# Kernel tuning notes

Hardware: AMD Instinct MI355X
Metric: run time of the kernel (lower is better)

## Reference

```python
import jax, jax.numpy as jnp
import numpy as np

N_NODES = 20000
N_EDGES = 320000
IN_F = 256
OUT_F = 64
HEADS = 4
ALPHA = 0.1  # leaky_relu negative slope


def setup_inputs() -> dict:
    key = jax.random.key(0)
    ks = jax.random.split(key, 8)
    return {
        "input1": jax.random.normal(ks[0], (N_NODES, IN_F), jnp.float32),
        "input2": jax.random.normal(ks[1], (N_NODES, IN_F), jnp.float32),
        # per-head params: Ws maps source feats -> target_out, Wt maps target feats -> source_out
        "Ws": jax.random.normal(ks[2], (HEADS, IN_F, OUT_F), jnp.float32) * 0.06,
        "Wt": jax.random.normal(ks[3], (HEADS, IN_F, OUT_F), jnp.float32) * 0.06,
        "a1": jax.random.normal(ks[4], (HEADS, 2 * OUT_F), jnp.float32) * 0.1,
        "a2": jax.random.normal(ks[5], (HEADS, 2 * OUT_F), jnp.float32) * 0.1,
        # COO nonzeros of A_opt [n_target, n_source]
        "tgt_idx": jax.random.randint(ks[6], (N_EDGES,), 0, N_NODES),
        "src_idx": jax.random.randint(ks[7], (N_EDGES,), 0, N_NODES),
    }


def _segment_softmax(scores, seg, num_segments):
    m = jax.lax.stop_gradient(jax.ops.segment_max(scores, seg, num_segments=num_segments))
    w = jnp.exp(scores - m[seg])
    d = jax.ops.segment_sum(w, seg, num_segments=num_segments)
    d = jnp.where(d == 0, 1.0, d)
    return w / d[seg]


def _head(x1, x2, Ws, Wt, a1, a2, src, tgt, n_s, n_t):
    s = x1 @ Ws  # [n_s, OUT_F]  messages source -> target
    t = x2 @ Wt  # [n_t, OUT_F]  messages target -> source
    out = Ws.shape[1]
    # edge score e = leaky_relu(a^T [s_src || t_tgt]); split a to avoid edge-level concat
    e1 = jax.nn.leaky_relu((s @ a1[:out])[src] + (t @ a1[out:])[tgt], ALPHA)
    e2 = jax.nn.leaky_relu((s @ a2[:out])[src] + (t @ a2[out:])[tgt], ALPHA)
    alpha_ts = _segment_softmax(e1, tgt, n_t)  # softmax over sources per target
    alpha_st = _segment_softmax(e2, src, n_s)  # softmax over targets per source
    h_ts = jax.ops.segment_sum(alpha_ts[:, None] * s[src], tgt, num_segments=n_t)
    h_st = jax.ops.segment_sum(alpha_st[:, None] * t[tgt], src, num_segments=n_s)
    return jax.nn.elu(h_st), jax.nn.elu(h_ts)  # concat=True -> ELU per head


def reference(input1, input2, Ws, Wt, a1, a2, tgt_idx, src_idx):
    n_s, n_t = input1.shape[0], input2.shape[0]
    head_fn = jax.vmap(
        lambda W1, W2, v1, v2: _head(input1, input2, W1, W2, v1, v2, src_idx, tgt_idx, n_s, n_t)
    )
    h_st, h_ts = head_fn(Ws, Wt, a1, a2)  # each [H, n, OUT_F]
    h_st = jnp.transpose(h_st, (1, 0, 2)).reshape(n_s, -1)  # concat heads
    h_ts = jnp.transpose(h_ts, (1, 0, 2)).reshape(n_t, -1)
    return h_st, h_ts
```

## Files before the change

### kernel.cpp

```cpp
#include <hip/hip_runtime.h>
#include <math.h>

#define N_NODES 20000
#define N_EDGES 320000
#define IN_F 256
#define OUT_F 64
#define HEADS 4
#define NCOL 256
#define LRELU_ALPHA 0.1f
#define ELL_CAP 64

#define SCAT_BLOCKS 640
#define SCAT_THREADS (SCAT_BLOCKS * 256)

#define WRES_BLOCKS 128
#define LDS_STRIDE 264

typedef __attribute__((ext_vector_type(8))) short short8;
typedef __attribute__((ext_vector_type(4))) float floatx4;

__device__ __forceinline__ float lrelu(float x) {
    return x > 0.f ? x : LRELU_ALPHA * x;
}
__device__ __forceinline__ unsigned short f2bf(float f) {
    unsigned int u = __float_as_uint(f);
    u = (u + 0x7FFF + ((u >> 16) & 1)) >> 16;
    return (unsigned short)u;
}
__device__ __forceinline__ float bf2f(unsigned short u) {
    return __uint_as_float(((unsigned int)u) << 16);
}

__global__ __launch_bounds__(256) void prep_w_kernel(
    const float* __restrict__ Ws, const float* __restrict__ Wt,
    unsigned short* __restrict__ Wsb, unsigned short* __restrict__ Wtb,
    int* __restrict__ cnt)
{
    const int gid = blockIdx.x * 256 + threadIdx.x;

    for (int i = gid; i < 2 * N_NODES; i += 16384) cnt[i] = 0;

    const int mat = gid >> 13;
    const int r   = gid & 8191;
    const int kc  = r >> 8;
    const int c   = r & 255;
    const float* W    = mat ? Wt : Ws;
    unsigned short* O = mat ? Wtb : Wsb;
    const int h = c >> 6, j = c & 63;
    const int k0 = kc * 8;
    unsigned short v[8] __attribute__((aligned(16)));
#pragma unroll
    for (int i = 0; i < 8; ++i)
        v[i] = f2bf(W[(size_t)h * (IN_F * OUT_F) + (size_t)(k0 + i) * OUT_F + j]);
    *(uint4*)(O + (size_t)c * IN_F + k0) = *(const uint4*)v;
}

__global__ __launch_bounds__(256) void scatter_kernel(
    const int* __restrict__ src, const int* __restrict__ tgt,
    int* __restrict__ cnt_t, int* __restrict__ cnt_s,
    unsigned short* __restrict__ elist_t, unsigned short* __restrict__ elist_s)
{
    const int e0 = blockIdx.x * 256 + threadIdx.x;
    const int e1 = e0 + SCAT_THREADS;
    const bool h1 = e1 < N_EDGES;

    int s0 = src[e0], t0 = tgt[e0];
    int s1 = 0, t1 = 0;
    if (h1) { s1 = src[e1]; t1 = tgt[e1]; }

    int p0 = atomicAdd(&cnt_t[t0], 1);
    int q0 = atomicAdd(&cnt_s[s0], 1);
    int p1 = 0, q1 = 0;
    if (h1) {
        p1 = atomicAdd(&cnt_t[t1], 1);
        q1 = atomicAdd(&cnt_s[s1], 1);
    }

    if (p0 < ELL_CAP) elist_t[t0 * ELL_CAP + p0] = (unsigned short)s0;
    if (q0 < ELL_CAP) elist_s[s0 * ELL_CAP + q0] = (unsigned short)t0;
    if (h1) {
        if (p1 < ELL_CAP) elist_t[t1 * ELL_CAP + p1] = (unsigned short)s1;
        if (q1 < ELL_CAP) elist_s[s1 * ELL_CAP + q1] = (unsigned short)t1;
    }
}

__global__ __launch_bounds__(512, 2) void gemm_wres_kernel(
    const float* __restrict__ A0, const unsigned short* __restrict__ Wb0,
    const float* __restrict__ A1, const unsigned short* __restrict__ Wb1,
    unsigned short* __restrict__ C0, unsigned short* __restrict__ C1,
    const float* __restrict__ a1, const float* __restrict__ a2,
    float* __restrict__ ss1, float* __restrict__ ss2,
    float* __restrict__ tt1, float* __restrict__ tt2)
{
    const int tid = threadIdx.x;
    const float* A           = (blockIdx.y == 0) ? A0 : A1;
    const unsigned short* Wb = (blockIdx.y == 0) ? Wb0 : Wb1;
    unsigned short* C        = (blockIdx.y == 0) ? C0 : C1;

    __shared__ __align__(16) unsigned short Bl[256][LDS_STRIDE];

    for (int i = tid; i < 8192; i += 512) {
        const int n  = i >> 5;
        const int kc = (i & 31) << 3;
        *(uint4*)&Bl[n][kc] = *(const uint4*)(Wb + (size_t)n * IN_F + kc);
    }
    __syncthreads();

    const int lane = tid & 63;
    const int w    = tid >> 6;
    const int quad = lane >> 4;
    const int l15  = lane & 15;
    const int slot = blockIdx.x * 8 + w;

    const int off_aj = (blockIdx.y == 0) ? 0 : 64;
    float* o1 = (blockIdx.y == 0) ? ss1 : tt1;
    float* o2 = (blockIdx.y == 0) ? ss2 : tt2;

    for (int g = slot; g < 1250; g += 1024) {
        const float* arow = A + (size_t)(g * 16 + l15) * IN_F + quad * 8;

        short8 af[8];
#pragma unroll
        for (int kk = 0; kk < 8; ++kk) {
            float4 u = *(const float4*)(arow + kk * 32);
            float4 v = *(const float4*)(arow + kk * 32 + 4);
            short8 t;
            t[0] = (short)f2bf(u.x); t[1] = (short)f2bf(u.y);
            t[2] = (short)f2bf(u.z); t[3] = (short)f2bf(u.w);
            t[4] = (short)f2bf(v.x); t[5] = (short)f2bf(v.y);
            t[6] = (short)f2bf(v.z); t[7] = (short)f2bf(v.w);
            af[kk] = t;
        }

        floatx4 acc[16];
#pragma unroll
        for (int c = 0; c < 16; ++c) acc[c] = (floatx4){0.f, 0.f, 0.f, 0.f};

#pragma unroll
        for (int kk = 0; kk < 8; ++kk) {
#pragma unroll
            for (int c = 0; c < 16; ++c) {
                short8 bfrag = *(const short8*)&Bl[c * 16 + l15][kk * 32 + quad * 8];
                acc[c] = __builtin_amdgcn_mfma_f32_16x16x32_bf16(af[kk], bfrag, acc[c], 0, 0, 0);
            }
        }

#pragma unroll
        for (int c = 0; c < 16; ++c) {
            const int col = c * 16 + l15;
#pragma unroll
            for (int r = 0; r < 4; ++r) {
                const int m = g * 16 + quad * 4 + r;
                C[(size_t)m * NCOL + col] = f2bf(acc[c][r]);
            }
        }

        float p1[4][4] = {{0.f,0.f,0.f,0.f},{0.f,0.f,0.f,0.f},{0.f,0.f,0.f,0.f},{0.f,0.f,0.f,0.f}};
        float p2[4][4] = {{0.f,0.f,0.f,0.f},{0.f,0.f,0.f,0.f},{0.f,0.f,0.f,0.f},{0.f,0.f,0.f,0.f}};
#pragma unroll
        for (int c = 0; c < 16; ++c) {
            const int hh = c >> 2;
            const int jj = (c & 3) * 16 + l15;
            const float w1 = a1[hh * 128 + off_aj + jj];
            const float w2 = a2[hh * 128 + off_aj + jj];
#pragma unroll
            for (int r = 0; r < 4; ++r) {
                p1[hh][r] += acc[c][r] * w1;
                p2[hh][r] += acc[c][r] * w2;
            }
        }
#pragma unroll
        for (int m = 1; m < 16; m <<= 1) {
#pragma unroll
            for (int hh = 0; hh < 4; ++hh)
#pragma unroll
                for (int r = 0; r < 4; ++r) {
                    p1[hh][r] += __shfl_xor(p1[hh][r], m, 64);
                    p2[hh][r] += __shfl_xor(p2[hh][r], m, 64);
                }
        }
        if (l15 == 0) {
#pragma unroll
            for (int r = 0; r < 4; ++r) {
                const int m = g * 16 + quad * 4 + r;
#pragma unroll
                for (int hh = 0; hh < 4; ++hh) {
                    o1[m * HEADS + hh] = p1[hh][r];
                    o2[m * HEADS + hh] = p2[hh][r];
                }
            }
        }
    }
}

__global__ __launch_bounds__(256) void agg_kernel(
    const int* __restrict__ cnt_t, const unsigned short* __restrict__ elist_t,
    const int* __restrict__ cnt_s, const unsigned short* __restrict__ elist_s,
    const float* __restrict__ ss1, const float* __restrict__ ss2,
    const float* __restrict__ tt1, const float* __restrict__ tt2,
    const unsigned short* __restrict__ s_bf, const unsigned short* __restrict__ t_bf,
    float* __restrict__ h_st, float* __restrict__ h_ts)
{
    const int wave = threadIdx.x >> 6;
    const int lane = threadIdx.x & 63;
    const int n    = blockIdx.x * 4 + wave;
    const int dir  = blockIdx.y;
    const int h    = lane >> 4;
    const int coff = lane * 4;

    const int*            cnt   = dir ? cnt_s   : cnt_t;
    const unsigned short* list  = dir ? elist_s : elist_t;
    const unsigned short* table = dir ? t_bf    : s_bf;
    const float*          nsc   = dir ? ss2     : tt1;
    const float*          esc   = dir ? tt2     : ss1;
    float*                outp  = dir ? h_st    : h_ts;

    const float base = nsc[n * HEADS + h];
    int deg = cnt[n];
    if (deg > ELL_CAP) deg = ELL_CAP;
    const int b0 = n * ELL_CAP, b1 = b0 + deg;

    float4 acc = make_float4(0.f, 0.f, 0.f, 0.f);
    float den = 0.f;

    int p = b0;
    for (; p + 3 < b1; p += 4) {
        int m0 = list[p],     m1 = list[p + 1];
        int m2 = list[p + 2], m3 = list[p + 3];
        float e0 = esc[m0 * HEADS + h], e1 = esc[m1 * HEADS + h];
        float e2 = esc[m2 * HEADS + h], e3 = esc[m3 * HEADS + h];
        ushort4 r0 = *(const ushort4*)(table + (size_t)m0 * NCOL + coff);
        ushort4 r1 = *(const ushort4*)(table + (size_t)m1 * NCOL + coff);
        ushort4 r2 = *(const ushort4*)(table + (size_t)m2 * NCOL + coff);
        ushort4 r3 = *(const ushort4*)(table + (size_t)m3 * NCOL + coff);
        float w0 = __expf(lrelu(e0 + base));
        float w1 = __expf(lrelu(e1 + base));
        float w2 = __expf(lrelu(e2 + base));
        float w3 = __expf(lrelu(e3 + base));
        den += (w0 + w1) + (w2 + w3);
        acc.x += (w0 * bf2f(r0.x) + w1 * bf2f(r1.x)) + (w2 * bf2f(r2.x) + w3 * bf2f(r3.x));
        acc.y += (w0 * bf2f(r0.y) + w1 * bf2f(r1.y)) + (w2 * bf2f(r2.y) + w3 * bf2f(r3.y));
        acc.z += (w0 * bf2f(r0.z) + w1 * bf2f(r1.z)) + (w2 * bf2f(r2.z) + w3 * bf2f(r3.z));
        acc.w += (w0 * bf2f(r0.w) + w1 * bf2f(r1.w)) + (w2 * bf2f(r2.w) + w3 * bf2f(r3.w));
    }
    for (; p < b1; ++p) {
        int m0 = list[p];
        float w0 = __expf(lrelu(esc[m0 * HEADS + h] + base));
        ushort4 r0 = *(const ushort4*)(table + (size_t)m0 * NCOL + coff);
        den += w0;
        acc.x += w0 * bf2f(r0.x);
        acc.y += w0 * bf2f(r0.y);
        acc.z += w0 * bf2f(r0.z);
        acc.w += w0 * bf2f(r0.w);
    }

    if (den == 0.f) den = 1.f;
    float inv = 1.f / den;
    float4 r;
    r.x = acc.x * inv; r.y = acc.y * inv; r.z = acc.z * inv; r.w = acc.w * inv;
    r.x = (r.x > 0.f) ? r.x : expm1f(r.x);
    r.y = (r.y > 0.f) ? r.y : expm1f(r.y);
    r.z = (r.z > 0.f) ? r.z : expm1f(r.z);
    r.w = (r.w > 0.f) ? r.w : expm1f(r.w);
    *(float4*)(outp + (size_t)n * NCOL + coff) = r;
}

extern "C" void kernel_launch(void* const* d_in, const int* in_sizes, int n_in,
                              void* d_out, int out_size, void* d_ws, size_t ws_size,
                              hipStream_t stream)
{
    const float* input1 = (const float*)d_in[0];
    const float* input2 = (const float*)d_in[1];
    const float* Ws     = (const float*)d_in[2];
    const float* Wt     = (const float*)d_in[3];
    const float* a1     = (const float*)d_in[4];
    const float* a2     = (const float*)d_in[5];
    const int*   tgt    = (const int*)d_in[6];
    const int*   src    = (const int*)d_in[7];

    float* out  = (float*)d_out;
    float* h_st = out;
    float* h_ts = out + (size_t)N_NODES * NCOL;

    unsigned short* s_bf = (unsigned short*)d_ws;
    unsigned short* t_bf = s_bf + (size_t)N_NODES * NCOL;
    unsigned short* Wsb  = t_bf + (size_t)N_NODES * NCOL;
    unsigned short* Wtb  = Wsb + 256 * 256;
    float* ss1  = (float*)(Wtb + 256 * 256);
    float* ss2  = ss1 + N_NODES * HEADS;
    float* tt1  = ss2 + N_NODES * HEADS;
    float* tt2  = tt1 + N_NODES * HEADS;
    int*   cnt_t = (int*)(tt2 + N_NODES * HEADS);
    int*   cnt_s = cnt_t + N_NODES;
    unsigned short* elist_t = (unsigned short*)(cnt_s + N_NODES);
    unsigned short* elist_s = elist_t + (size_t)N_NODES * ELL_CAP;

    prep_w_kernel<<<64, 256, 0, stream>>>(Ws, Wt, Wsb, Wtb, cnt_t);

    scatter_kernel<<<SCAT_BLOCKS, 256, 0, stream>>>(src, tgt, cnt_t, cnt_s,
                                                    elist_t, elist_s);

    dim3 ggrid(WRES_BLOCKS, 2);
    gemm_wres_kernel<<<ggrid, 512, 0, stream>>>(input1, Wsb, input2, Wtb,
                                                s_bf, t_bf, a1, a2,
                                                ss1, ss2, tt1, tt2);

    dim3 agrid(N_NODES / 4, 2);
    agg_kernel<<<agrid, 256, 0, stream>>>(cnt_t, elist_t, cnt_s, elist_s,
                                          ss1, ss2, tt1, tt2, s_bf, t_bf, h_st, h_ts);
}
```

Before: 193.6 us.

## Restructure GEMM to 1024-thread blocks and split aggregation by head slices

The GEMM kernel moves to 1024-thread blocks with one 16-row tile per wave. It splits the K dimension into two halves so the loads of the second half overlap the MFMAs of the first. The aggregation kernel now assigns each block a (direction, head) slice over a contiguous node range. Within each wave the four quads split a node's edges and are combined with shuffles, which raises memory-level parallelism per edge list. In exchange there is more reduction overhead, only a quarter of lanes store results, and the 1024-thread launch bound may cause register pressure or spills.

```diff
diff --git a/kernel.cpp b/kernel.cpp
--- a/kernel.cpp
+++ b/kernel.cpp
@@ -15,6 +15,8 @@
 
 #define WRES_BLOCKS 128
 #define LDS_STRIDE 264
+
+#define AGG_BLOCKS 2048
 
 typedef __attribute__((ext_vector_type(8))) short short8;
 typedef __attribute__((ext_vector_type(4))) float floatx4;
@@ -84,7 +86,7 @@
     }
 }
 
-__global__ __launch_bounds__(512, 2) void gemm_wres_kernel(
+__global__ __launch_bounds__(1024, 4) void gemm_wres_kernel(
     const float* __restrict__ A0, const unsigned short* __restrict__ Wb0,
     const float* __restrict__ A1, const unsigned short* __restrict__ Wb1,
     unsigned short* __restrict__ C0, unsigned short* __restrict__ C1,
@@ -99,7 +101,7 @@
 
     __shared__ __align__(16) unsigned short Bl[256][LDS_STRIDE];
 
-    for (int i = tid; i < 8192; i += 512) {
+    for (int i = tid; i < 8192; i += 1024) {
         const int n  = i >> 5;
         const int kc = (i & 31) << 3;
         *(uint4*)&Bl[n][kc] = *(const uint4*)(Wb + (size_t)n * IN_F + kc);
@@ -110,84 +112,113 @@
     const int w    = tid >> 6;
     const int quad = lane >> 4;
     const int l15  = lane & 15;
-    const int slot = blockIdx.x * 8 + w;
+    const int g    = blockIdx.x * 16 + w;
+
+    if (g >= 1250) return;
+
+    const float* arow = A + (size_t)(g * 16 + l15) * IN_F + quad * 8;
+
+    float4 ua[8];
+#pragma unroll
+    for (int kk = 0; kk < 4; ++kk) {
+        ua[2 * kk]     = *(const float4*)(arow + kk * 32);
+        ua[2 * kk + 1] = *(const float4*)(arow + kk * 32 + 4);
+    }
+    short8 af[4];
+#pragma unroll
+    for (int kk = 0; kk < 4; ++kk) {
+        short8 t;
+        t[0] = (short)f2bf(ua[2 * kk].x);     t[1] = (short)f2bf(ua[2 * kk].y);
+        t[2] = (short)f2bf(ua[2 * kk].z);     t[3] = (short)f2bf(ua[2 * kk].w);
+        t[4] = (short)f2bf(ua[2 * kk + 1].x); t[5] = (short)f2bf(ua[2 * kk + 1].y);
+        t[6] = (short)f2bf(ua[2 * kk + 1].z); t[7] = (short)f2bf(ua[2 * kk + 1].w);
+        af[kk] = t;
+    }
+
+    float4 ub[8];
+#pragma unroll
+    for (int kk = 0; kk < 4; ++kk) {
+        ub[2 * kk]     = *(const float4*)(arow + (kk + 4) * 32);
+        ub[2 * kk + 1] = *(const float4*)(arow + (kk + 4) * 32 + 4);
+    }
+
+    floatx4 acc[16];
+#pragma unroll
+    for (int c = 0; c < 16; ++c) acc[c] = (floatx4){0.f, 0.f, 0.f, 0.f};
+
+#pragma unroll
+    for (int kk = 0; kk < 4; ++kk) {
+#pragma unroll
+        for (int c = 0; c < 16; ++c) {
+            short8 bfrag = *(const short8*)&Bl[c * 16 + l15][kk * 32 + quad * 8];
+            acc[c] = __builtin_amdgcn_mfma_f32_16x16x32_bf16(af[kk], bfrag, acc[c], 0, 0, 0);
+        }
+    }
+
+#pragma unroll
+    for (int kk = 0; kk < 4; ++kk) {
+        short8 t;
+        t[0] = (short)f2bf(ub[2 * kk].x);     t[1] = (short)f2bf(ub[2 * kk].y);
+        t[2] = (short)f2bf(ub[2 * kk].z);     t[3] = (short)f2bf(ub[2 * kk].w);
+        t[4] = (short)f2bf(ub[2 * kk + 1].x); t[5] = (short)f2bf(ub[2 * kk + 1].y);
+        t[6] = (short)f2bf(ub[2 * kk + 1].z); t[7] = (short)f2bf(ub[2 * kk + 1].w);
+        af[kk] = t;
+    }
+#pragma unroll
+    for (int kk = 0; kk < 4; ++kk) {
+#pragma unroll
+        for (int c = 0; c < 16; ++c) {
+            short8 bfrag = *(const short8*)&Bl[c * 16 + l15][(kk + 4) * 32 + quad * 8];
+            acc[c] = __builtin_amdgcn_mfma_f32_16x16x32_bf16(af[kk], bfrag, acc[c], 0, 0, 0);
+        }
+    }
+
+#pragma unroll
+    for (int c = 0; c < 16; ++c) {
+        const int col = c * 16 + l15;
+#pragma unroll
+        for (int r = 0; r < 4; ++r) {
+            const int m = g * 16 + quad * 4 + r;
+            C[(size_t)m * NCOL + col] = f2bf(acc[c][r]);
+        }
+    }
 
     const int off_aj = (blockIdx.y == 0) ? 0 : 64;
     float* o1 = (blockIdx.y == 0) ? ss1 : tt1;
     float* o2 = (blockIdx.y == 0) ? ss2 : tt2;
 
-    for (int g = slot; g < 1250; g += 1024) {
-        const float* arow = A + (size_t)(g * 16 + l15) * IN_F + quad * 8;
-
-        short8 af[8];
-#pragma unroll
-        for (int kk = 0; kk < 8; ++kk) {
-            float4 u = *(const float4*)(arow + kk * 32);
-            float4 v = *(const float4*)(arow + kk * 32 + 4);
-            short8 t;
-            t[0] = (short)f2bf(u.x); t[1] = (short)f2bf(u.y);
-            t[2] = (short)f2bf(u.z); t[3] = (short)f2bf(u.w);
-            t[4] = (short)f2bf(v.x); t[5] = (short)f2bf(v.y);
-            t[6] = (short)f2bf(v.z); t[7] = (short)f2bf(v.w);
-            af[kk] = t;
-        }
-
-        floatx4 acc[16];
-#pragma unroll
-        for (int c = 0; c < 16; ++c) acc[c] = (floatx4){0.f, 0.f, 0.f, 0.f};
-
-#pragma unroll
-        for (int kk = 0; kk < 8; ++kk) {
-#pragma unroll
-            for (int c = 0; c < 16; ++c) {
-                short8 bfrag = *(const short8*)&Bl[c * 16 + l15][kk * 32 + quad * 8];
-                acc[c] = __builtin_amdgcn_mfma_f32_16x16x32_bf16(af[kk], bfrag, acc[c], 0, 0, 0);
+    float p1[4][4] = {{0.f,0.f,0.f,0.f},{0.f,0.f,0.f,0.f},{0.f,0.f,0.f,0.f},{0.f,0.f,0.f,0.f}};
+    float p2[4][4] = {{0.f,0.f,0.f,0.f},{0.f,0.f,0.f,0.f},{0.f,0.f,0.f,0.f},{0.f,0.f,0.f,0.f}};
+#pragma unroll
+    for (int c = 0; c < 16; ++c) {
+        const int hh = c >> 2;
+        const int jj = (c & 3) * 16 + l15;
+        const float w1 = a1[hh * 128 + off_aj + jj];
+        const float w2 = a2[hh * 128 + off_aj + jj];
+#pragma unroll
+        for (int r = 0; r < 4; ++r) {
+            p1[hh][r] += acc[c][r] * w1;
+            p2[hh][r] += acc[c][r] * w2;
+        }
+    }
+#pragma unroll
+    for (int m = 1; m < 16; m <<= 1) {
+#pragma unroll
+        for (int hh = 0; hh < 4; ++hh)
+#pragma unroll
+            for (int r = 0; r < 4; ++r) {
+                p1[hh][r] += __shfl_xor(p1[hh][r], m, 64);
+                p2[hh][r] += __shfl_xor(p2[hh][r], m, 64);
             }
-        }
-
-#pragma unroll
-        for (int c = 0; c < 16; ++c) {
-            const int col = c * 16 + l15;
-#pragma unroll
-            for (int r = 0; r < 4; ++r) {
-                const int m = g * 16 + quad * 4 + r;
-                C[(size_t)m * NCOL + col] = f2bf(acc[c][r]);
-            }
-        }
-
-        float p1[4][4] = {{0.f,0.f,0.f,0.f},{0.f,0.f,0.f,0.f},{0.f,0.f,0.f,0.f},{0.f,0.f,0.f,0.f}};
-        float p2[4][4] = {{0.f,0.f,0.f,0.f},{0.f,0.f,0.f,0.f},{0.f,0.f,0.f,0.f},{0.f,0.f,0.f,0.f}};
-#pragma unroll
-        for (int c = 0; c < 16; ++c) {
-            const int hh = c >> 2;
-            const int jj = (c & 3) * 16 + l15;
-            const float w1 = a1[hh * 128 + off_aj + jj];
-            const float w2 = a2[hh * 128 + off_aj + jj];
-#pragma unroll
-            for (int r = 0; r < 4; ++r) {
-                p1[hh][r] += acc[c][r] * w1;
-                p2[hh][r] += acc[c][r] * w2;
-            }
-        }
-#pragma unroll
-        for (int m = 1; m < 16; m <<= 1) {
-#pragma unroll
-            for (int hh = 0; hh < 4; ++hh)
-#pragma unroll
-                for (int r = 0; r < 4; ++r) {
-                    p1[hh][r] += __shfl_xor(p1[hh][r], m, 64);
-                    p2[hh][r] += __shfl_xor(p2[hh][r], m, 64);
-                }
-        }
-        if (l15 == 0) {
-#pragma unroll
-            for (int r = 0; r < 4; ++r) {
-                const int m = g * 16 + quad * 4 + r;
-#pragma unroll
-                for (int hh = 0; hh < 4; ++hh) {
-                    o1[m * HEADS + hh] = p1[hh][r];
-                    o2[m * HEADS + hh] = p2[hh][r];
-                }
+    }
+    if (l15 == 0) {
+#pragma unroll
+        for (int r = 0; r < 4; ++r) {
+            const int m = g * 16 + quad * 4 + r;
+#pragma unroll
+            for (int hh = 0; hh < 4; ++hh) {
+                o1[m * HEADS + hh] = p1[hh][r];
+                o2[m * HEADS + hh] = p2[hh][r];
             }
         }
     }
@@ -201,12 +232,16 @@
     const unsigned short* __restrict__ s_bf, const unsigned short* __restrict__ t_bf,
     float* __restrict__ h_st, float* __restrict__ h_ts)
 {
-    const int wave = threadIdx.x >> 6;
-    const int lane = threadIdx.x & 63;
-    const int n    = blockIdx.x * 4 + wave;
-    const int dir  = blockIdx.y;
-    const int h    = lane >> 4;
-    const int coff = lane * 4;
+    const int b     = blockIdx.x;
+    const int slice = b & 7;
+    const int dir   = slice >> 2;
+    const int h     = slice & 3;
+    const int idx   = b >> 3;
+    const int wave  = threadIdx.x >> 6;
+    const int lane  = threadIdx.x & 63;
+    const int quad  = lane >> 4;
+    const int l15   = lane & 15;
+    const int coff  = h * 64 + l15 * 4;
 
     const int*            cnt   = dir ? cnt_s   : cnt_t;
     const unsigned short* list  = dir ? elist_s : elist_t;
@@ -215,54 +250,66 @@
     const float*          esc   = dir ? tt2     : ss1;
     float*                outp  = dir ? h_st    : h_ts;
 
-    const float base = nsc[n * HEADS + h];
-    int deg = cnt[n];
-    if (deg > ELL_CAP) deg = ELL_CAP;
-    const int b0 = n * ELL_CAP, b1 = b0 + deg;
-
-    float4 acc = make_float4(0.f, 0.f, 0.f, 0.f);
-    float den = 0.f;
-
-    int p = b0;
-    for (; p + 3 < b1; p += 4) {
-        int m0 = list[p],     m1 = list[p + 1];
-        int m2 = list[p + 2], m3 = list[p + 3];
-        float e0 = esc[m0 * HEADS + h], e1 = esc[m1 * HEADS + h];
-        float e2 = esc[m2 * HEADS + h], e3 = esc[m3 * HEADS + h];
-        ushort4 r0 = *(const ushort4*)(table + (size_t)m0 * NCOL + coff);
-        ushort4 r1 = *(const ushort4*)(table + (size_t)m1 * NCOL + coff);
-        ushort4 r2 = *(const ushort4*)(table + (size_t)m2 * NCOL + coff);
-        ushort4 r3 = *(const ushort4*)(table + (size_t)m3 * NCOL + coff);
-        float w0 = __expf(lrelu(e0 + base));
-        float w1 = __expf(lrelu(e1 + base));
-        float w2 = __expf(lrelu(e2 + base));
-        float w3 = __expf(lrelu(e3 + base));
-        den += (w0 + w1) + (w2 + w3);
-        acc.x += (w0 * bf2f(r0.x) + w1 * bf2f(r1.x)) + (w2 * bf2f(r2.x) + w3 * bf2f(r3.x));
-        acc.y += (w0 * bf2f(r0.y) + w1 * bf2f(r1.y)) + (w2 * bf2f(r2.y) + w3 * bf2f(r3.y));
-        acc.z += (w0 * bf2f(r0.z) + w1 * bf2f(r1.z)) + (w2 * bf2f(r2.z) + w3 * bf2f(r3.z));
-        acc.w += (w0 * bf2f(r0.w) + w1 * bf2f(r1.w)) + (w2 * bf2f(r2.w) + w3 * bf2f(r3.w));
-    }
-    for (; p < b1; ++p) {
-        int m0 = list[p];
-        float w0 = __expf(lrelu(esc[m0 * HEADS + h] + base));
-        ushort4 r0 = *(const ushort4*)(table + (size_t)m0 * NCOL + coff);
-        den += w0;
-        acc.x += w0 * bf2f(r0.x);
-        acc.y += w0 * bf2f(r0.y);
-        acc.z += w0 * bf2f(r0.z);
-        acc.w += w0 * bf2f(r0.w);
-    }
-
-    if (den == 0.f) den = 1.f;
-    float inv = 1.f / den;
-    float4 r;
-    r.x = acc.x * inv; r.y = acc.y * inv; r.z = acc.z * inv; r.w = acc.w * inv;
-    r.x = (r.x > 0.f) ? r.x : expm1f(r.x);
-    r.y = (r.y > 0.f) ? r.y : expm1f(r.y);
-    r.z = (r.z > 0.f) ? r.z : expm1f(r.z);
-    r.w = (r.w > 0.f) ? r.w : expm1f(r.w);
-    *(float4*)(outp + (size_t)n * NCOL + coff) = r;
+    const int nstart = (idx * N_NODES) >> 8;
+    const int nend   = ((idx + 1) * N_NODES) >> 8;
+
+    for (int n = nstart + wave; n < nend; n += 4) {
+        const float base = nsc[n * HEADS + h];
+        int deg = cnt[n];
+        if (deg > ELL_CAP) deg = ELL_CAP;
+        const unsigned short* lp = list + n * ELL_CAP;
+
+        float4 acc = make_float4(0.f, 0.f, 0.f, 0.f);
+        float den = 0.f;
+
+        int p = quad;
+        for (; p + 4 < deg; p += 8) {
+            int m0 = lp[p], m1 = lp[p + 4];
+            float e0 = esc[m0 * HEADS + h];
+            float e1 = esc[m1 * HEADS + h];
+            ushort4 r0 = *(const ushort4*)(table + (size_t)m0 * NCOL + coff);
+            ushort4 r1 = *(const ushort4*)(table + (size_t)m1 * NCOL + coff);
+            float w0 = __expf(lrelu(e0 + base));
+            float w1 = __expf(lrelu(e1 + base));
+            den += w0 + w1;
+            acc.x += w0 * bf2f(r0.x) + w1 * bf2f(r1.x);
+            acc.y += w0 * bf2f(r0.y) + w1 * bf2f(r1.y);
+            acc.z += w0 * bf2f(r0.z) + w1 * bf2f(r1.z);
+            acc.w += w0 * bf2f(r0.w) + w1 * bf2f(r1.w);
+        }
+        if (p < deg) {
+            int m0 = lp[p];
+            float w0 = __expf(lrelu(esc[m0 * HEADS + h] + base));
+            ushort4 r0 = *(const ushort4*)(table + (size_t)m0 * NCOL + coff);
+            den += w0;
+            acc.x += w0 * bf2f(r0.x);
+            acc.y += w0 * bf2f(r0.y);
+            acc.z += w0 * bf2f(r0.z);
+            acc.w += w0 * bf2f(r0.w);
+        }
+
+#pragma unroll
+        for (int msk = 16; msk < 64; msk <<= 1) {
+            den   += __shfl_xor(den,   msk, 64);
+            acc.x += __shfl_xor(acc.x, msk, 64);
+            acc.y += __shfl_xor(acc.y, msk, 64);
+            acc.z += __shfl_xor(acc.z, msk, 64);
+            acc.w += __shfl_xor(acc.w, msk, 64);
+        }
+
+        if (quad == 0) {
+            if (den == 0.f) den = 1.f;
+            float inv = 1.f / den;
+            float4 r;
+            r.x = acc.x * inv; r.y = acc.y * inv;
+            r.z = acc.z * inv; r.w = acc.w * inv;
+            r.x = (r.x > 0.f) ? r.x : expm1f(r.x);
+            r.y = (r.y > 0.f) ? r.y : expm1f(r.y);
+            r.z = (r.z > 0.f) ? r.z : expm1f(r.z);
+            r.w = (r.w > 0.f) ? r.w : expm1f(r.w);
+            *(float4*)(outp + (size_t)n * NCOL + coff) = r;
+        }
+    }
 }
 
 extern "C" void kernel_launch(void* const* d_in, const int* in_sizes, int n_in,
@@ -301,11 +348,10 @@
                                                     elist_t, elist_s);
 
     dim3 ggrid(WRES_BLOCKS, 2);
-    gemm_wres_kernel<<<ggrid, 512, 0, stream>>>(input1, Wsb, input2, Wtb,
-                                                s_bf, t_bf, a1, a2,
-                                                ss1, ss2, tt1, tt2);
-
-    dim3 agrid(N_NODES / 4, 2);
-    agg_kernel<<<agrid, 256, 0, stream>>>(cnt_t, elist_t, cnt_s, elist_s,
-                                          ss1, ss2, tt1, tt2, s_bf, t_bf, h_st, h_ts);
-}
+    gemm_wres_kernel<<<ggrid, 1024, 0, stream>>>(input1, Wsb, input2, Wtb,
+                                                 s_bf, t_bf, a1, a2,
+                                                 ss1, ss2, tt1, tt2);
+
+    agg_kernel<<<AGG_BLOCKS, 256, 0, stream>>>(cnt_t, elist_t, cnt_s, elist_s,
+                                               ss1, ss2, tt1, tt2, s_bf, t_bf, h_st, h_ts);
+}
```

After: 219.2 us. 13.2% more time.
